# Optimization experiments

Hardware: AMD Instinct MI355X
Metric: run time of the kernel (lower is better)

## Reference

```python
import jax, jax.numpy as jnp
import numpy as np

T, H, E, I, K = 2048, 2048, 8, 2048, 2


def setup_inputs() -> dict:
    key = jax.random.key(0)
    ks = jax.random.split(key, 6)
    s_in = 1.0 / np.sqrt(H)
    s_mid = 1.0 / np.sqrt(I)
    return {
        "hidden_states": jax.random.normal(ks[0], (T, H), jnp.float32),
        "router_logits": jax.random.normal(ks[1], (T, E), jnp.float32),
        "per_expert_scale": jax.random.uniform(ks[2], (E,), jnp.float32, 0.5, 1.5),
        "w_gate": jax.random.normal(ks[3], (E, H, I), jnp.float32) * s_in,
        "w_up": jax.random.normal(ks[4], (E, H, I), jnp.float32) * s_in,
        "w_down": jax.random.normal(ks[5], (E, I, H), jnp.float32) * s_mid,
    }


def _route(router_logits, per_expert_scale):
    # Gemma4 routing: topk over logits, softmax over ALL experts,
    # renormalize over selected experts, fold in per-expert scale.
    _, topk_ids = jax.lax.top_k(router_logits, K)              # [T, K]
    probs = jax.nn.softmax(router_logits, axis=-1)             # [T, E]
    topk_probs = jnp.take_along_axis(probs, topk_ids, axis=-1)  # [T, K]
    renorm = jnp.sum(topk_probs, axis=-1, keepdims=True)
    renorm = jnp.where(renorm > 0.0, renorm, 1.0)
    topk_weights = topk_probs / renorm
    topk_weights = topk_weights * per_expert_scale[topk_ids]
    return topk_weights.astype(jnp.float32), topk_ids.astype(jnp.int32)


def reference(hidden_states, router_logits, per_expert_scale, w_gate, w_up, w_down):
    topk_weights, topk_ids = _route(router_logits, per_expert_scale)
    # dense combine weights [T, E] (zero outside top-k slots)
    combine = jnp.zeros((T, E), jnp.float32)
    combine = combine.at[jnp.arange(T)[:, None], topk_ids].set(topk_weights)
    # gated gelu MLP per expert, dense over experts, weighted combine
    g = jax.nn.gelu(jnp.einsum('th,ehi->tei', hidden_states, w_gate), approximate=True)
    u = jnp.einsum('th,ehi->tei', hidden_states, w_up)
    expert_out = jnp.einsum('tei,eih->teh', g * u, w_down)      # [T, E, H]
    out = jnp.einsum('te,teh->th', combine, expert_out)
    return out
```

## Files before the change

kernel.cpp:

```cpp
#include <hip/hip_runtime.h>
#include <hip/hip_bf16.h>

#define TT 2048
#define HD 2048
#define ID 2048
#define NE 8

typedef __attribute__((ext_vector_type(8))) short short8;
typedef __attribute__((ext_vector_type(4))) float f4;

__device__ __forceinline__ unsigned short b16(float f){
  union { __hip_bfloat16 b; unsigned short u; } x;
  x.b = __float2bfloat16(f);
  return x.u;
}
__device__ __forceinline__ unsigned pk2(float lo, float hi){
  return (unsigned)b16(lo) | ((unsigned)b16(hi) << 16);
}
__device__ __forceinline__ float gelu_t(float x){
  float y = 0.7978845608028654f * (x + 0.044715f * x * x * x);
  float t = 1.0f - 2.0f / (__expf(2.0f * y) + 1.0f);
  return 0.5f * x * (1.0f + t);
}
__device__ __forceinline__ void glds16(const void* g, void* l){
  __builtin_amdgcn_global_load_lds(
      (const __attribute__((address_space(1))) unsigned*)g,
      (__attribute__((address_space(3))) unsigned*)l, 16, 0, 0);
}
__device__ __forceinline__ void softbar(){
  asm volatile("s_waitcnt lgkmcnt(0)" ::: "memory");
  __builtin_amdgcn_s_barrier();
  __builtin_amdgcn_sched_barrier(0);
}
__device__ __forceinline__ int swzB2(int np){ return (((np >> 2) & 7) ^ ((np & 3) << 1)) & 7; }

__global__ void k_cvtx(const float* __restrict__ X, __hip_bfloat16* __restrict__ Xb){
  int i = blockIdx.x * 256 + threadIdx.x;
  const f4* src = (const f4*)X + (size_t)i * 2;
  f4 a = src[0], b = src[1];
  uint4 o = { pk2(a[0],a[1]), pk2(a[2],a[3]), pk2(b[0],b[1]), pk2(b[2],b[3]) };
  ((uint4*)Xb)[i] = o;
}

__global__ void k_route(const float* __restrict__ lg, const float* __restrict__ sc,
                        int* __restrict__ rid, float* __restrict__ rw){
  int t = blockIdx.x * blockDim.x + threadIdx.x;
  if (t >= TT) return;
  float l[NE];
#pragma unroll
  for (int e = 0; e < NE; e++) l[e] = lg[t * NE + e];
  float mx = l[0];
#pragma unroll
  for (int e = 1; e < NE; e++) mx = fmaxf(mx, l[e]);
  float p[NE];
#pragma unroll
  for (int e = 0; e < NE; e++) p[e] = __expf(l[e] - mx);
  int i0 = 0; float b0 = l[0];
#pragma unroll
  for (int e = 1; e < NE; e++) if (l[e] > b0){ b0 = l[e]; i0 = e; }
  int i1 = -1; float b1 = -1e30f;
#pragma unroll
  for (int e = 0; e < NE; e++) if (e != i0 && l[e] > b1){ b1 = l[e]; i1 = e; }
  float p0 = p[i0], p1 = p[i1];
  float rn = p0 + p1; rn = (rn > 0.f) ? rn : 1.f;
  rw[t*2]   = p0 / rn * sc[i0];
  rw[t*2+1] = p1 / rn * sc[i1];
  rid[t*2]  = i0;
  rid[t*2+1]= i1;
}

__global__ void k_lists(const int* __restrict__ rid, const float* __restrict__ rw,
                        int* __restrict__ row_tok, float* __restrict__ row_w,
                        int* __restrict__ off){
  int lane = threadIdx.x;
  int ids[64]; float wv[64];
#pragma unroll
  for (int i = 0; i < 64; i++) ids[i] = rid[i * 64 + lane];
#pragma unroll
  for (int i = 0; i < 64; i++) wv[i] = rw[i * 64 + lane];
  int cnt[NE];
#pragma unroll
  for (int e = 0; e < NE; e++) cnt[e] = 0;
#pragma unroll
  for (int i = 0; i < 64; i++){
#pragma unroll
    for (int e = 0; e < NE; e++)
      cnt[e] += __popcll(__ballot(ids[i] == e));
  }
  int offs[NE + 1]; offs[0] = 0;
#pragma unroll
  for (int e = 0; e < NE; e++) offs[e + 1] = offs[e] + cnt[e];
  if (lane == 0){
#pragma unroll
    for (int e = 0; e <= NE; e++) off[e] = offs[e];
  }
  int run[NE];
#pragma unroll
  for (int e = 0; e < NE; e++) run[e] = offs[e];
  unsigned long long ltm = (1ULL << lane) - 1ULL;
#pragma unroll
  for (int i = 0; i < 64; i++){
    int id = ids[i];
    int tok = (i * 64 + lane) >> 1;
#pragma unroll
    for (int e = 0; e < NE; e++){
      unsigned long long m = __ballot(id == e);
      if (id == e){
        int pos = run[e] + __popcll(m & ltm);
        row_tok[pos] = tok;
        row_w[pos]   = wv[i];
      }
      run[e] += __popcll(m);
    }
  }
}


__global__ __launch_bounds__(256, 3)
void k_gu_f(const __hip_bfloat16* __restrict__ Xb, const float* __restrict__ Wg,
            const float* __restrict__ Wu, const int* __restrict__ row_tok,
            const float* __restrict__ row_w, const int* __restrict__ off,
            __hip_bfloat16* __restrict__ hbuf){
  __shared__ __align__(16) char sA[2][16384];
  __shared__ __align__(16) char sB[16384];
  __shared__ int s_tok[128];
  __shared__ float s_w[128];

  const int bid = blockIdx.x;
  const int e  = bid & 7;
  const int t  = bid >> 3;
  const int mt = t % 5;
  const int nt = t / 5;
  const int o0 = off[e], cnt = off[e + 1] - o0;
  if (mt * 128 >= cnt) return;
  const int p0 = o0 + mt * 128;
  const int cntL = min(128, cnt - mt * 128);
  const int tid = threadIdx.x;
  const int wid = tid >> 6, lane = tid & 63;

  if (tid < 128){
    int p = min(p0 + tid, TT*2 - 1);
    s_tok[tid] = row_tok[p];
    s_w[tid]   = row_w[p];
  }
  __syncthreads();

  const int sw = (((lane & 7) ^ (lane >> 3)) & 7) << 4;
  const char* asrc[4];
#pragma unroll
  for (int i = 0; i < 4; i++){
    int r = (wid * 4 + i) * 8 + (lane >> 3);
    asrc[i] = (const char*)Xb + (size_t)s_tok[r] * 4096 + sw;
  }
  const int m2 = tid >> 7, tt = tid & 127;
  const int n0 = (tt & 15) * 4;
  const int s0 = tt >> 4;
  const float* wsrc = (m2 ? Wu : Wg) + (size_t)e * HD * ID
                    + (size_t)(s0 * 8) * ID + (size_t)nt * 64 + n0;
  int bw[4];
#pragma unroll
  for (int j = 0; j < 4; j++){
    int n  = n0 + j;
    int np = (n >> 5) * 64 + (n & 31) + m2 * 32;
    bw[j] = np * 128 + (((s0 ^ swzB2(np)) & 7) << 4);
  }
  const int wm = wid >> 1, wn = wid & 1;
  const int kg = lane >> 4, ln = lane & 15;
  int aoff[4], boff[4];
#pragma unroll
  for (int f = 0; f < 4; f++){
    int m = wm * 64 + f * 16 + ln;
    aoff[f] = m * 128 + (((kg ^ (m & 7)) & 7) << 4);
    int n = wn * 64 + f * 16 + ln;
    boff[f] = n * 128 + (((kg ^ swzB2(n)) & 7) << 4);
  }

  f4 acc[4][4];
#pragma unroll
  for (int a = 0; a < 4; a++)
#pragma unroll
    for (int b = 0; b < 4; b++) acc[a][b] = f4{0,0,0,0};

#pragma unroll
  for (int i = 0; i < 4; i++) glds16(asrc[i], &sA[0][0] + (wid * 4 + i) * 1024);
  f4 rk[8];
#pragma unroll
  for (int i = 0; i < 8; i++) rk[i] = *(const f4*)(wsrc + (size_t)i * ID);

  for (int kt = 0; kt < 32; ++kt){
    softbar();
#pragma unroll
    for (int j = 0; j < 4; j++){
      *(uint4*)(sB + bw[j]) = uint4{ pk2(rk[0][j], rk[1][j]), pk2(rk[2][j], rk[3][j]),
                                     pk2(rk[4][j], rk[5][j]), pk2(rk[6][j], rk[7][j]) };
    }
    __builtin_amdgcn_sched_barrier(0);
    if (kt + 1 < 32){
      const int _o = (kt + 1) * 128;
      char* dst = &sA[(kt + 1) & 1][0] + (wid * 4) * 1024;
#pragma unroll
      for (int i = 0; i < 4; i++) glds16(asrc[i] + _o, dst + i * 1024);
    }
    __builtin_amdgcn_sched_barrier(0);
    if (kt + 1 < 32){
      const float* p = wsrc + (size_t)(kt + 1) * 64 * ID;
#pragma unroll
      for (int i = 0; i < 8; i++) rk[i] = *(const f4*)(p + (size_t)i * ID);
    }
    __builtin_amdgcn_sched_barrier(0);
    asm volatile("s_waitcnt lgkmcnt(0)" ::: "memory");
    __builtin_amdgcn_s_barrier();
    __builtin_amdgcn_sched_barrier(0);
    const char* A = &sA[kt & 1][0];
#pragma unroll
    for (int ks = 0; ks < 2; ks++){
      const int kx = ks * 64;
      short8 af[4], bf[4];
#pragma unroll
      for (int f = 0; f < 4; f++) af[f] = *(const short8*)(A + (aoff[f] ^ kx));
#pragma unroll
      for (int f = 0; f < 4; f++) bf[f] = *(const short8*)(sB + (boff[f] ^ kx));
#pragma unroll
      for (int fn = 0; fn < 4; fn++)
#pragma unroll
        for (int fm = 0; fm < 4; fm++)
          acc[fm][fn] = __builtin_amdgcn_mfma_f32_16x16x32_bf16(af[fm], bf[fn], acc[fm][fn], 0, 0, 0);
    }
  }
#pragma unroll
  for (int fm = 0; fm < 4; fm++){
#pragma unroll
    for (int r = 0; r < 4; r++){
      int row = wm * 64 + fm * 16 + (lane >> 4) * 4 + r;
      if (row < cntL){
        float w = s_w[row];
        size_t base = (size_t)(p0 + row) * ID + (size_t)nt * 64 + wn * 32 + ln;
#pragma unroll
        for (int fn = 0; fn < 2; fn++){
          float g = acc[fm][fn][r];
          float u = acc[fm][fn + 2][r];
          hbuf[base + fn * 16] = __float2bfloat16(w * gelu_t(g) * u);
        }
      }
    }
  }
}

__global__ __launch_bounds__(256, 3)
void k_dn_f(const __hip_bfloat16* __restrict__ hbuf, const float* __restrict__ Wd,
            const int* __restrict__ row_tok, const int* __restrict__ off,
            float* __restrict__ out){
  __shared__ __align__(16) char sA[2][16384];
  __shared__ __align__(16) char sB[16384];
  __shared__ int s_tok[128];

  const int bid = blockIdx.x;
  const int e  = bid & 7;
  const int t  = bid >> 3;
  const int mt = t % 5;
  const int nt = t / 5;
  const int o0 = off[e], cnt = off[e + 1] - o0;
  if (mt * 128 >= cnt) return;
  const int p0 = o0 + mt * 128;
  const int cntL = min(128, cnt - mt * 128);
  const int tid = threadIdx.x;
  const int wid = tid >> 6, lane = tid & 63;

  if (tid < 128){
    int p = min(p0 + tid, TT*2 - 1);
    s_tok[tid] = row_tok[p];
  }
  __syncthreads();

  const int sw = (((lane & 7) ^ (lane >> 3)) & 7) << 4;
  const char* asrc[4];
#pragma unroll
  for (int i = 0; i < 4; i++){
    int r = (wid * 4 + i) * 8 + (lane >> 3);
    int p = min(p0 + r, TT*2 - 1);
    asrc[i] = (const char*)hbuf + (size_t)p * 4096 + sw;
  }
  const int n0 = (tid & 31) * 4;
  const int s0 = tid >> 5;
  const float* wsrc = Wd + (size_t)e * ID * HD + (size_t)(s0 * 8) * HD + (size_t)nt * 128 + n0;
  int bw[4];
#pragma unroll
  for (int j = 0; j < 4; j++){
    int np = n0 + j;
    bw[j] = np * 128 + (((s0 ^ swzB2(np)) & 7) << 4);
  }
  const int wm = wid >> 1, wn = wid & 1;
  const int kg = lane >> 4, ln = lane & 15;
  int aoff[4], boff[4];
#pragma unroll
  for (int f = 0; f < 4; f++){
    int m = wm * 64 + f * 16 + ln;
    aoff[f] = m * 128 + (((kg ^ (m & 7)) & 7) << 4);
    int n = wn * 64 + f * 16 + ln;
    boff[f] = n * 128 + (((kg ^ swzB2(n)) & 7) << 4);
  }

  f4 acc[4][4];
#pragma unroll
  for (int a = 0; a < 4; a++)
#pragma unroll
    for (int b = 0; b < 4; b++) acc[a][b] = f4{0,0,0,0};

#pragma unroll
  for (int i = 0; i < 4; i++) glds16(asrc[i], &sA[0][0] + (wid * 4 + i) * 1024);
  f4 rk[8];
#pragma unroll
  for (int i = 0; i < 8; i++) rk[i] = *(const f4*)(wsrc + (size_t)i * HD);

  for (int kt = 0; kt < 32; ++kt){
    softbar();
#pragma unroll
    for (int j = 0; j < 4; j++){
      *(uint4*)(sB + bw[j]) = uint4{ pk2(rk[0][j], rk[1][j]), pk2(rk[2][j], rk[3][j]),
                                     pk2(rk[4][j], rk[5][j]), pk2(rk[6][j], rk[7][j]) };
    }
    __builtin_amdgcn_sched_barrier(0);
    if (kt + 1 < 32){
      const int _o = (kt + 1) * 128;
      char* dst = &sA[(kt + 1) & 1][0] + (wid * 4) * 1024;
#pragma unroll
      for (int i = 0; i < 4; i++) glds16(asrc[i] + _o, dst + i * 1024);
    }
    __builtin_amdgcn_sched_barrier(0);
    if (kt + 1 < 32){
      const float* p = wsrc + (size_t)(kt + 1) * 64 * HD;
#pragma unroll
      for (int i = 0; i < 8; i++) rk[i] = *(const f4*)(p + (size_t)i * HD);
    }
    __builtin_amdgcn_sched_barrier(0);
    asm volatile("s_waitcnt lgkmcnt(0)" ::: "memory");
    __builtin_amdgcn_s_barrier();
    __builtin_amdgcn_sched_barrier(0);
    const char* A = &sA[kt & 1][0];
#pragma unroll
    for (int ks = 0; ks < 2; ks++){
      const int kx = ks * 64;
      short8 af[4], bf[4];
#pragma unroll
      for (int f = 0; f < 4; f++) af[f] = *(const short8*)(A + (aoff[f] ^ kx));
#pragma unroll
      for (int f = 0; f < 4; f++) bf[f] = *(const short8*)(sB + (boff[f] ^ kx));
#pragma unroll
      for (int fn = 0; fn < 4; fn++)
#pragma unroll
        for (int fm = 0; fm < 4; fm++)
          acc[fm][fn] = __builtin_amdgcn_mfma_f32_16x16x32_bf16(af[fm], bf[fn], acc[fm][fn], 0, 0, 0);
    }
  }
#pragma unroll
  for (int fm = 0; fm < 4; fm++){
#pragma unroll
    for (int r = 0; r < 4; r++){
      int row = wm * 64 + fm * 16 + (lane >> 4) * 4 + r;
      if (row < cntL){
        int tok = s_tok[row];
        float* ob = out + (size_t)tok * HD + (size_t)nt * 128 + wn * 64 + ln;
#pragma unroll
        for (int fn = 0; fn < 4; fn++)
          atomicAdd(ob + fn * 16, acc[fm][fn][r]);
      }
    }
  }
}

extern "C" void kernel_launch(void* const* d_in, const int* in_sizes, int n_in,
                              void* d_out, int out_size, void* d_ws, size_t ws_size,
                              hipStream_t stream){
  (void)in_sizes; (void)n_in; (void)out_size; (void)ws_size;
  const float* X  = (const float*)d_in[0];
  const float* RL = (const float*)d_in[1];
  const float* SC = (const float*)d_in[2];
  const float* Wg = (const float*)d_in[3];
  const float* Wu = (const float*)d_in[4];
  const float* Wd = (const float*)d_in[5];
  float* out = (float*)d_out;

  char* ws = (char*)d_ws;
  int*   rid     = (int*)(ws);
  float* rw      = (float*)(ws + 16384);
  int*   row_tok = (int*)(ws + 32768);
  float* row_w   = (float*)(ws + 49152);
  int*   off     = (int*)(ws + 65536);
  __hip_bfloat16* hbuf = (__hip_bfloat16*)(ws + 66560);
  __hip_bfloat16* Xb   = (__hip_bfloat16*)(ws + 66560 + 16777216ull);

  hipMemsetAsync(d_out, 0, (size_t)TT * HD * sizeof(float), stream);
  k_cvtx <<<2048, 256, 0, stream>>>(X, Xb);
  k_route<<<TT / 256, 256, 0, stream>>>(RL, SC, rid, rw);
  k_lists<<<1, 64, 0, stream>>>(rid, rw, row_tok, row_w, off);
  k_gu_f<<<1280, 256, 0, stream>>>(Xb, Wg, Wu, row_tok, row_w, off, hbuf);
  k_dn_f<<< 640, 256, 0, stream>>>(hbuf, Wd, row_tok, off, out);
}
```

Before: 302.1 us.

## Make expert GEMM kernels persistent with an atomic tile work queue

Both expert GEMM kernels become persistent. A fixed grid of 768 blocks pulls tile indices from a global atomic counter, which k_lists resets each call, instead of launching one block per potential tile and early-exiting empty ones. This is meant to cut the cost of launching and retiring blocks for empty tiles, and to balance uneven per-expert token counts across CUs. In exchange it adds an atomic and a barrier per tile. The shared s_tile slot can be overwritten by thread 0 before slower waves have read it on the empty-tile path, which risks waves disagreeing on the tile or mismatched barriers.

```diff
diff --git a/kernel.cpp b/kernel.cpp
--- a/kernel.cpp
+++ b/kernel.cpp
@@ -71,8 +71,9 @@
 
 __global__ void k_lists(const int* __restrict__ rid, const float* __restrict__ rw,
                         int* __restrict__ row_tok, float* __restrict__ row_w,
-                        int* __restrict__ off){
+                        int* __restrict__ off, int* __restrict__ qcnt){
   int lane = threadIdx.x;
+  if (lane < 2) qcnt[lane] = 0;
   int ids[64]; float wv[64];
 #pragma unroll
   for (int i = 0; i < 64; i++) ids[i] = rid[i * 64 + lane];
@@ -120,43 +121,20 @@
 void k_gu_f(const __hip_bfloat16* __restrict__ Xb, const float* __restrict__ Wg,
             const float* __restrict__ Wu, const int* __restrict__ row_tok,
             const float* __restrict__ row_w, const int* __restrict__ off,
-            __hip_bfloat16* __restrict__ hbuf){
+            int* __restrict__ qcnt, __hip_bfloat16* __restrict__ hbuf){
   __shared__ __align__(16) char sA[2][16384];
   __shared__ __align__(16) char sB[16384];
   __shared__ int s_tok[128];
   __shared__ float s_w[128];
-
-  const int bid = blockIdx.x;
-  const int e  = bid & 7;
-  const int t  = bid >> 3;
-  const int mt = t % 5;
-  const int nt = t / 5;
-  const int o0 = off[e], cnt = off[e + 1] - o0;
-  if (mt * 128 >= cnt) return;
-  const int p0 = o0 + mt * 128;
-  const int cntL = min(128, cnt - mt * 128);
+  __shared__ int s_tile;
+
   const int tid = threadIdx.x;
   const int wid = tid >> 6, lane = tid & 63;
 
-  if (tid < 128){
-    int p = min(p0 + tid, TT*2 - 1);
-    s_tok[tid] = row_tok[p];
-    s_w[tid]   = row_w[p];
-  }
-  __syncthreads();
-
   const int sw = (((lane & 7) ^ (lane >> 3)) & 7) << 4;
-  const char* asrc[4];
-#pragma unroll
-  for (int i = 0; i < 4; i++){
-    int r = (wid * 4 + i) * 8 + (lane >> 3);
-    asrc[i] = (const char*)Xb + (size_t)s_tok[r] * 4096 + sw;
-  }
   const int m2 = tid >> 7, tt = tid & 127;
   const int n0 = (tt & 15) * 4;
   const int s0 = tt >> 4;
-  const float* wsrc = (m2 ? Wu : Wg) + (size_t)e * HD * ID
-                    + (size_t)(s0 * 8) * ID + (size_t)nt * 64 + n0;
   int bw[4];
 #pragma unroll
   for (int j = 0; j < 4; j++){
@@ -175,71 +153,102 @@
     boff[f] = n * 128 + (((kg ^ swzB2(n)) & 7) << 4);
   }
 
-  f4 acc[4][4];
-#pragma unroll
-  for (int a = 0; a < 4; a++)
-#pragma unroll
-    for (int b = 0; b < 4; b++) acc[a][b] = f4{0,0,0,0};
-
-#pragma unroll
-  for (int i = 0; i < 4; i++) glds16(asrc[i], &sA[0][0] + (wid * 4 + i) * 1024);
-  f4 rk[8];
-#pragma unroll
-  for (int i = 0; i < 8; i++) rk[i] = *(const f4*)(wsrc + (size_t)i * ID);
-
-  for (int kt = 0; kt < 32; ++kt){
-    softbar();
-#pragma unroll
-    for (int j = 0; j < 4; j++){
-      *(uint4*)(sB + bw[j]) = uint4{ pk2(rk[0][j], rk[1][j]), pk2(rk[2][j], rk[3][j]),
-                                     pk2(rk[4][j], rk[5][j]), pk2(rk[6][j], rk[7][j]) };
-    }
-    __builtin_amdgcn_sched_barrier(0);
-    if (kt + 1 < 32){
-      const int _o = (kt + 1) * 128;
-      char* dst = &sA[(kt + 1) & 1][0] + (wid * 4) * 1024;
-#pragma unroll
-      for (int i = 0; i < 4; i++) glds16(asrc[i] + _o, dst + i * 1024);
-    }
-    __builtin_amdgcn_sched_barrier(0);
-    if (kt + 1 < 32){
-      const float* p = wsrc + (size_t)(kt + 1) * 64 * ID;
-#pragma unroll
-      for (int i = 0; i < 8; i++) rk[i] = *(const f4*)(p + (size_t)i * ID);
-    }
-    __builtin_amdgcn_sched_barrier(0);
-    asm volatile("s_waitcnt lgkmcnt(0)" ::: "memory");
-    __builtin_amdgcn_s_barrier();
-    __builtin_amdgcn_sched_barrier(0);
-    const char* A = &sA[kt & 1][0];
-#pragma unroll
-    for (int ks = 0; ks < 2; ks++){
-      const int kx = ks * 64;
-      short8 af[4], bf[4];
-#pragma unroll
-      for (int f = 0; f < 4; f++) af[f] = *(const short8*)(A + (aoff[f] ^ kx));
-#pragma unroll
-      for (int f = 0; f < 4; f++) bf[f] = *(const short8*)(sB + (boff[f] ^ kx));
-#pragma unroll
-      for (int fn = 0; fn < 4; fn++)
-#pragma unroll
-        for (int fm = 0; fm < 4; fm++)
-          acc[fm][fn] = __builtin_amdgcn_mfma_f32_16x16x32_bf16(af[fm], bf[fn], acc[fm][fn], 0, 0, 0);
-    }
-  }
-#pragma unroll
-  for (int fm = 0; fm < 4; fm++){
-#pragma unroll
-    for (int r = 0; r < 4; r++){
-      int row = wm * 64 + fm * 16 + (lane >> 4) * 4 + r;
-      if (row < cntL){
-        float w = s_w[row];
-        size_t base = (size_t)(p0 + row) * ID + (size_t)nt * 64 + wn * 32 + ln;
-#pragma unroll
-        for (int fn = 0; fn < 2; fn++){
-          float g = acc[fm][fn][r];
-          float u = acc[fm][fn + 2][r];
-          hbuf[base + fn * 16] = __float2bfloat16(w * gelu_t(g) * u);
+  for (;;){
+    if (tid == 0) s_tile = atomicAdd(qcnt, 1);
+    __syncthreads();
+    const int tile = s_tile;
+    if (tile >= 1280) break;
+    const int e  = tile & 7;
+    const int t  = tile >> 3;
+    const int mt = t % 5;
+    const int nt = t / 5;
+    const int o0 = off[e], cnt = off[e + 1] - o0;
+    if (mt * 128 >= cnt) continue;
+    const int p0 = o0 + mt * 128;
+    const int cntL = min(128, cnt - mt * 128);
+
+    if (tid < 128){
+      int p = min(p0 + tid, TT*2 - 1);
+      s_tok[tid] = row_tok[p];
+      s_w[tid]   = row_w[p];
+    }
+    __syncthreads();
+
+    const char* asrc[4];
+#pragma unroll
+    for (int i = 0; i < 4; i++){
+      int r = (wid * 4 + i) * 8 + (lane >> 3);
+      asrc[i] = (const char*)Xb + (size_t)s_tok[r] * 4096 + sw;
+    }
+    const float* wsrc = (m2 ? Wu : Wg) + (size_t)e * HD * ID
+                      + (size_t)(s0 * 8) * ID + (size_t)nt * 64 + n0;
+
+    f4 acc[4][4];
+#pragma unroll
+    for (int a = 0; a < 4; a++)
+#pragma unroll
+      for (int b = 0; b < 4; b++) acc[a][b] = f4{0,0,0,0};
+
+#pragma unroll
+    for (int i = 0; i < 4; i++) glds16(asrc[i], &sA[0][0] + (wid * 4 + i) * 1024);
+    f4 rk[8];
+#pragma unroll
+    for (int i = 0; i < 8; i++) rk[i] = *(const f4*)(wsrc + (size_t)i * ID);
+
+    for (int kt = 0; kt < 32; ++kt){
+      softbar();
+#pragma unroll
+      for (int j = 0; j < 4; j++){
+        *(uint4*)(sB + bw[j]) = uint4{ pk2(rk[0][j], rk[1][j]), pk2(rk[2][j], rk[3][j]),
+                                       pk2(rk[4][j], rk[5][j]), pk2(rk[6][j], rk[7][j]) };
+      }
+      __builtin_amdgcn_sched_barrier(0);
+      if (kt + 1 < 32){
+        const int _o = (kt + 1) * 128;
+        char* dst = &sA[(kt + 1) & 1][0] + (wid * 4) * 1024;
+#pragma unroll
+        for (int i = 0; i < 4; i++) glds16(asrc[i] + _o, dst + i * 1024);
+      }
+      __builtin_amdgcn_sched_barrier(0);
+      if (kt + 1 < 32){
+        const float* p = wsrc + (size_t)(kt + 1) * 64 * ID;
+#pragma unroll
+        for (int i = 0; i < 8; i++) rk[i] = *(const f4*)(p + (size_t)i * ID);
+      }
+      __builtin_amdgcn_sched_barrier(0);
+      asm volatile("s_waitcnt lgkmcnt(0)" ::: "memory");
+      __builtin_amdgcn_s_barrier();
+      __builtin_amdgcn_sched_barrier(0);
+      const char* A = &sA[kt & 1][0];
+#pragma unroll
+      for (int ks = 0; ks < 2; ks++){
+        const int kx = ks * 64;
+        short8 af[4], bf[4];
+#pragma unroll
+        for (int f = 0; f < 4; f++) af[f] = *(const short8*)(A + (aoff[f] ^ kx));
+#pragma unroll
+        for (int f = 0; f < 4; f++) bf[f] = *(const short8*)(sB + (boff[f] ^ kx));
+#pragma unroll
+        for (int fn = 0; fn < 4; fn++)
+#pragma unroll
+          for (int fm = 0; fm < 4; fm++)
+            acc[fm][fn] = __builtin_amdgcn_mfma_f32_16x16x32_bf16(af[fm], bf[fn], acc[fm][fn], 0, 0, 0);
+      }
+    }
+#pragma unroll
+    for (int fm = 0; fm < 4; fm++){
+#pragma unroll
+      for (int r = 0; r < 4; r++){
+        int row = wm * 64 + fm * 16 + (lane >> 4) * 4 + r;
+        if (row < cntL){
+          float w = s_w[row];
+          size_t base = (size_t)(p0 + row) * ID + (size_t)nt * 64 + wn * 32 + ln;
+#pragma unroll
+          for (int fn = 0; fn < 2; fn++){
+            float g = acc[fm][fn][r];
+            float u = acc[fm][fn + 2][r];
+            hbuf[base + fn * 16] = __float2bfloat16(w * gelu_t(g) * u);
+          }
         }
       }
     }
@@ -249,40 +258,18 @@
 __global__ __launch_bounds__(256, 3)
 void k_dn_f(const __hip_bfloat16* __restrict__ hbuf, const float* __restrict__ Wd,
             const int* __restrict__ row_tok, const int* __restrict__ off,
-            float* __restrict__ out){
+            int* __restrict__ qcnt, float* __restrict__ out){
   __shared__ __align__(16) char sA[2][16384];
   __shared__ __align__(16) char sB[16384];
   __shared__ int s_tok[128];
-
-  const int bid = blockIdx.x;
-  const int e  = bid & 7;
-  const int t  = bid >> 3;
-  const int mt = t % 5;
-  const int nt = t / 5;
-  const int o0 = off[e], cnt = off[e + 1] - o0;
-  if (mt * 128 >= cnt) return;
-  const int p0 = o0 + mt * 128;
-  const int cntL = min(128, cnt - mt * 128);
+  __shared__ int s_tile;
+
   const int tid = threadIdx.x;
   const int wid = tid >> 6, lane = tid & 63;
 
-  if (tid < 128){
-    int p = min(p0 + tid, TT*2 - 1);
-    s_tok[tid] = row_tok[p];
-  }
-  __syncthreads();
-
   const int sw = (((lane & 7) ^ (lane >> 3)) & 7) << 4;
-  const char* asrc[4];
-#pragma unroll
-  for (int i = 0; i < 4; i++){
-    int r = (wid * 4 + i) * 8 + (lane >> 3);
-    int p = min(p0 + r, TT*2 - 1);
-    asrc[i] = (const char*)hbuf + (size_t)p * 4096 + sw;
-  }
   const int n0 = (tid & 31) * 4;
   const int s0 = tid >> 5;
-  const float* wsrc = Wd + (size_t)e * ID * HD + (size_t)(s0 * 8) * HD + (size_t)nt * 128 + n0;
   int bw[4];
 #pragma unroll
   for (int j = 0; j < 4; j++){
@@ -300,69 +287,99 @@
     boff[f] = n * 128 + (((kg ^ swzB2(n)) & 7) << 4);
   }
 
-  f4 acc[4][4];
-#pragma unroll
-  for (int a = 0; a < 4; a++)
-#pragma unroll
-    for (int b = 0; b < 4; b++) acc[a][b] = f4{0,0,0,0};
-
-#pragma unroll
-  for (int i = 0; i < 4; i++) glds16(asrc[i], &sA[0][0] + (wid * 4 + i) * 1024);
-  f4 rk[8];
-#pragma unroll
-  for (int i = 0; i < 8; i++) rk[i] = *(const f4*)(wsrc + (size_t)i * HD);
-
-  for (int kt = 0; kt < 32; ++kt){
-    softbar();
-#pragma unroll
-    for (int j = 0; j < 4; j++){
-      *(uint4*)(sB + bw[j]) = uint4{ pk2(rk[0][j], rk[1][j]), pk2(rk[2][j], rk[3][j]),
-                                     pk2(rk[4][j], rk[5][j]), pk2(rk[6][j], rk[7][j]) };
-    }
-    __builtin_amdgcn_sched_barrier(0);
-    if (kt + 1 < 32){
-      const int _o = (kt + 1) * 128;
-      char* dst = &sA[(kt + 1) & 1][0] + (wid * 4) * 1024;
-#pragma unroll
-      for (int i = 0; i < 4; i++) glds16(asrc[i] + _o, dst + i * 1024);
-    }
-    __builtin_amdgcn_sched_barrier(0);
-    if (kt + 1 < 32){
-      const float* p = wsrc + (size_t)(kt + 1) * 64 * HD;
-#pragma unroll
-      for (int i = 0; i < 8; i++) rk[i] = *(const f4*)(p + (size_t)i * HD);
-    }
-    __builtin_amdgcn_sched_barrier(0);
-    asm volatile("s_waitcnt lgkmcnt(0)" ::: "memory");
-    __builtin_amdgcn_s_barrier();
-    __builtin_amdgcn_sched_barrier(0);
-    const char* A = &sA[kt & 1][0];
-#pragma unroll
-    for (int ks = 0; ks < 2; ks++){
-      const int kx = ks * 64;
-      short8 af[4], bf[4];
-#pragma unroll
-      for (int f = 0; f < 4; f++) af[f] = *(const short8*)(A + (aoff[f] ^ kx));
-#pragma unroll
-      for (int f = 0; f < 4; f++) bf[f] = *(const short8*)(sB + (boff[f] ^ kx));
-#pragma unroll
-      for (int fn = 0; fn < 4; fn++)
-#pragma unroll
-        for (int fm = 0; fm < 4; fm++)
-          acc[fm][fn] = __builtin_amdgcn_mfma_f32_16x16x32_bf16(af[fm], bf[fn], acc[fm][fn], 0, 0, 0);
-    }
-  }
-#pragma unroll
-  for (int fm = 0; fm < 4; fm++){
-#pragma unroll
-    for (int r = 0; r < 4; r++){
-      int row = wm * 64 + fm * 16 + (lane >> 4) * 4 + r;
-      if (row < cntL){
-        int tok = s_tok[row];
-        float* ob = out + (size_t)tok * HD + (size_t)nt * 128 + wn * 64 + ln;
+  for (;;){
+    if (tid == 0) s_tile = atomicAdd(qcnt + 1, 1);
+    __syncthreads();
+    const int tile = s_tile;
+    if (tile >= 640) break;
+    const int e  = tile & 7;
+    const int t  = tile >> 3;
+    const int mt = t % 5;
+    const int nt = t / 5;
+    const int o0 = off[e], cnt = off[e + 1] - o0;
+    if (mt * 128 >= cnt) continue;
+    const int p0 = o0 + mt * 128;
+    const int cntL = min(128, cnt - mt * 128);
+
+    if (tid < 128){
+      int p = min(p0 + tid, TT*2 - 1);
+      s_tok[tid] = row_tok[p];
+    }
+    __syncthreads();
+
+    const char* asrc[4];
+#pragma unroll
+    for (int i = 0; i < 4; i++){
+      int r = (wid * 4 + i) * 8 + (lane >> 3);
+      int p = min(p0 + r, TT*2 - 1);
+      asrc[i] = (const char*)hbuf + (size_t)p * 4096 + sw;
+    }
+    const float* wsrc = Wd + (size_t)e * ID * HD + (size_t)(s0 * 8) * HD + (size_t)nt * 128 + n0;
+
+    f4 acc[4][4];
+#pragma unroll
+    for (int a = 0; a < 4; a++)
+#pragma unroll
+      for (int b = 0; b < 4; b++) acc[a][b] = f4{0,0,0,0};
+
+#pragma unroll
+    for (int i = 0; i < 4; i++) glds16(asrc[i], &sA[0][0] + (wid * 4 + i) * 1024);
+    f4 rk[8];
+#pragma unroll
+    for (int i = 0; i < 8; i++) rk[i] = *(const f4*)(wsrc + (size_t)i * HD);
+
+    for (int kt = 0; kt < 32; ++kt){
+      softbar();
+#pragma unroll
+      for (int j = 0; j < 4; j++){
+        *(uint4*)(sB + bw[j]) = uint4{ pk2(rk[0][j], rk[1][j]), pk2(rk[2][j], rk[3][j]),
+                                       pk2(rk[4][j], rk[5][j]), pk2(rk[6][j], rk[7][j]) };
+      }
+      __builtin_amdgcn_sched_barrier(0);
+      if (kt + 1 < 32){
+        const int _o = (kt + 1) * 128;
+        char* dst = &sA[(kt + 1) & 1][0] + (wid * 4) * 1024;
+#pragma unroll
+        for (int i = 0; i < 4; i++) glds16(asrc[i] + _o, dst + i * 1024);
+      }
+      __builtin_amdgcn_sched_barrier(0);
+      if (kt + 1 < 32){
+        const float* p = wsrc + (size_t)(kt + 1) * 64 * HD;
+#pragma unroll
+        for (int i = 0; i < 8; i++) rk[i] = *(const f4*)(p + (size_t)i * HD);
+      }
+      __builtin_amdgcn_sched_barrier(0);
+      asm volatile("s_waitcnt lgkmcnt(0)" ::: "memory");
+      __builtin_amdgcn_s_barrier();
+      __builtin_amdgcn_sched_barrier(0);
+      const char* A = &sA[kt & 1][0];
+#pragma unroll
+      for (int ks = 0; ks < 2; ks++){
+        const int kx = ks * 64;
+        short8 af[4], bf[4];
+#pragma unroll
+        for (int f = 0; f < 4; f++) af[f] = *(const short8*)(A + (aoff[f] ^ kx));
+#pragma unroll
+        for (int f = 0; f < 4; f++) bf[f] = *(const short8*)(sB + (boff[f] ^ kx));
 #pragma unroll
         for (int fn = 0; fn < 4; fn++)
-          atomicAdd(ob + fn * 16, acc[fm][fn][r]);
+#pragma unroll
+          for (int fm = 0; fm < 4; fm++)
+            acc[fm][fn] = __builtin_amdgcn_mfma_f32_16x16x32_bf16(af[fm], bf[fn], acc[fm][fn], 0, 0, 0);
+      }
+    }
+#pragma unroll
+    for (int fm = 0; fm < 4; fm++){
+#pragma unroll
+      for (int r = 0; r < 4; r++){
+        int row = wm * 64 + fm * 16 + (lane >> 4) * 4 + r;
+        if (row < cntL){
+          int tok = s_tok[row];
+          float* ob = out + (size_t)tok * HD + (size_t)nt * 128 + wn * 64 + ln;
+#pragma unroll
+          for (int fn = 0; fn < 4; fn++)
+            atomicAdd(ob + fn * 16, acc[fm][fn][r]);
+        }
       }
     }
   }
@@ -386,13 +403,14 @@
   int*   row_tok = (int*)(ws + 32768);
   float* row_w   = (float*)(ws + 49152);
   int*   off     = (int*)(ws + 65536);
+  int*   qcnt    = (int*)(ws + 66048);
   __hip_bfloat16* hbuf = (__hip_bfloat16*)(ws + 66560);
   __hip_bfloat16* Xb   = (__hip_bfloat16*)(ws + 66560 + 16777216ull);
 
   hipMemsetAsync(d_out, 0, (size_t)TT * HD * sizeof(float), stream);
   k_cvtx <<<2048, 256, 0, stream>>>(X, Xb);
   k_route<<<TT / 256, 256, 0, stream>>>(RL, SC, rid, rw);
-  k_lists<<<1, 64, 0, stream>>>(rid, rw, row_tok, row_w, off);
-  k_gu_f<<<1280, 256, 0, stream>>>(Xb, Wg, Wu, row_tok, row_w, off, hbuf);
-  k_dn_f<<< 640, 256, 0, stream>>>(hbuf, Wd, row_tok, off, out);
-}
+  k_lists<<<1, 64, 0, stream>>>(rid, rw, row_tok, row_w, off, qcnt);
+  k_gu_f<<<768, 256, 0, stream>>>(Xb, Wg, Wu, row_tok, row_w, off, qcnt, hbuf);
+  k_dn_f<<<768, 256, 0, stream>>>(hbuf, Wd, row_tok, off, qcnt, out);
+}
```

Result: slower. 396.9 us (+31.4%).

## Double the M tile to 256 rows and single-buffer the activation tile

Applied to the files above, without the earlier changes.

Both expert GEMM kernels now cover 256 routed rows per block instead of 128, with 8x4 MFMA fragments per wave. Each expert needs 3 M tiles instead of 5, so the fp32 expert weights are read and converted to bf16 fewer times. The double-buffered A tile becomes one 32 KB buffer, loaded at the start of each k-step and waited on with a partial vmcnt that leaves the weight prefetch in flight. The costs are higher register pressure (launch bounds drop from 3 to 2 blocks per SM), less overlap of A loads with compute, and rows lost if any expert receives more than 768 assignments.

```diff
diff --git a/kernel.cpp b/kernel.cpp
--- a/kernel.cpp
+++ b/kernel.cpp
@@ -116,29 +116,29 @@
 }
 
 
-__global__ __launch_bounds__(256, 3)
+__global__ __launch_bounds__(256, 2)
 void k_gu_f(const __hip_bfloat16* __restrict__ Xb, const float* __restrict__ Wg,
             const float* __restrict__ Wu, const int* __restrict__ row_tok,
             const float* __restrict__ row_w, const int* __restrict__ off,
             __hip_bfloat16* __restrict__ hbuf){
-  __shared__ __align__(16) char sA[2][16384];
+  __shared__ __align__(16) char sA[32768];
   __shared__ __align__(16) char sB[16384];
-  __shared__ int s_tok[128];
-  __shared__ float s_w[128];
+  __shared__ int s_tok[256];
+  __shared__ float s_w[256];
 
   const int bid = blockIdx.x;
   const int e  = bid & 7;
   const int t  = bid >> 3;
-  const int mt = t % 5;
-  const int nt = t / 5;
+  const int mt = t % 3;
+  const int nt = t / 3;
   const int o0 = off[e], cnt = off[e + 1] - o0;
-  if (mt * 128 >= cnt) return;
-  const int p0 = o0 + mt * 128;
-  const int cntL = min(128, cnt - mt * 128);
+  if (mt * 256 >= cnt) return;
+  const int p0 = o0 + mt * 256;
+  const int cntL = min(256, cnt - mt * 256);
   const int tid = threadIdx.x;
   const int wid = tid >> 6, lane = tid & 63;
 
-  if (tid < 128){
+  {
     int p = min(p0 + tid, TT*2 - 1);
     s_tok[tid] = row_tok[p];
     s_w[tid]   = row_w[p];
@@ -146,10 +146,10 @@
   __syncthreads();
 
   const int sw = (((lane & 7) ^ (lane >> 3)) & 7) << 4;
-  const char* asrc[4];
-#pragma unroll
-  for (int i = 0; i < 4; i++){
-    int r = (wid * 4 + i) * 8 + (lane >> 3);
+  const char* asrc[8];
+#pragma unroll
+  for (int i = 0; i < 8; i++){
+    int r = (wid * 8 + i) * 8 + (lane >> 3);
     asrc[i] = (const char*)Xb + (size_t)s_tok[r] * 4096 + sw;
   }
   const int m2 = tid >> 7, tt = tid & 127;
@@ -166,29 +166,36 @@
   }
   const int wm = wid >> 1, wn = wid & 1;
   const int kg = lane >> 4, ln = lane & 15;
-  int aoff[4], boff[4];
+  int aoff[8], boff[4];
+#pragma unroll
+  for (int f = 0; f < 8; f++){
+    int m = wm * 128 + f * 16 + ln;
+    aoff[f] = m * 128 + (((kg ^ (m & 7)) & 7) << 4);
+  }
 #pragma unroll
   for (int f = 0; f < 4; f++){
-    int m = wm * 64 + f * 16 + ln;
-    aoff[f] = m * 128 + (((kg ^ (m & 7)) & 7) << 4);
     int n = wn * 64 + f * 16 + ln;
     boff[f] = n * 128 + (((kg ^ swzB2(n)) & 7) << 4);
   }
 
-  f4 acc[4][4];
-#pragma unroll
-  for (int a = 0; a < 4; a++)
+  f4 acc[8][4];
+#pragma unroll
+  for (int a = 0; a < 8; a++)
 #pragma unroll
     for (int b = 0; b < 4; b++) acc[a][b] = f4{0,0,0,0};
 
-#pragma unroll
-  for (int i = 0; i < 4; i++) glds16(asrc[i], &sA[0][0] + (wid * 4 + i) * 1024);
   f4 rk[8];
 #pragma unroll
   for (int i = 0; i < 8; i++) rk[i] = *(const f4*)(wsrc + (size_t)i * ID);
+  __builtin_amdgcn_sched_barrier(0);
 
   for (int kt = 0; kt < 32; ++kt){
     softbar();
+    { const int _o = kt * 128;
+#pragma unroll
+      for (int i = 0; i < 8; i++) glds16(asrc[i] + _o, sA + (wid * 8 + i) * 1024);
+    }
+    __builtin_amdgcn_sched_barrier(0);
 #pragma unroll
     for (int j = 0; j < 4; j++){
       *(uint4*)(sB + bw[j]) = uint4{ pk2(rk[0][j], rk[1][j]), pk2(rk[2][j], rk[3][j]),
@@ -196,42 +203,38 @@
     }
     __builtin_amdgcn_sched_barrier(0);
     if (kt + 1 < 32){
-      const int _o = (kt + 1) * 128;
-      char* dst = &sA[(kt + 1) & 1][0] + (wid * 4) * 1024;
-#pragma unroll
-      for (int i = 0; i < 4; i++) glds16(asrc[i] + _o, dst + i * 1024);
+      const float* p = wsrc + (size_t)(kt + 1) * 64 * ID;
+#pragma unroll
+      for (int i = 0; i < 8; i++) rk[i] = *(const f4*)(p + (size_t)i * ID);
     }
     __builtin_amdgcn_sched_barrier(0);
     if (kt + 1 < 32){
-      const float* p = wsrc + (size_t)(kt + 1) * 64 * ID;
-#pragma unroll
-      for (int i = 0; i < 8; i++) rk[i] = *(const f4*)(p + (size_t)i * ID);
-    }
-    __builtin_amdgcn_sched_barrier(0);
-    asm volatile("s_waitcnt lgkmcnt(0)" ::: "memory");
+      asm volatile("s_waitcnt vmcnt(8) lgkmcnt(0)" ::: "memory");
+    } else {
+      asm volatile("s_waitcnt vmcnt(0) lgkmcnt(0)" ::: "memory");
+    }
     __builtin_amdgcn_s_barrier();
     __builtin_amdgcn_sched_barrier(0);
-    const char* A = &sA[kt & 1][0];
 #pragma unroll
     for (int ks = 0; ks < 2; ks++){
       const int kx = ks * 64;
-      short8 af[4], bf[4];
-#pragma unroll
-      for (int f = 0; f < 4; f++) af[f] = *(const short8*)(A + (aoff[f] ^ kx));
+      short8 bf[4];
 #pragma unroll
       for (int f = 0; f < 4; f++) bf[f] = *(const short8*)(sB + (boff[f] ^ kx));
 #pragma unroll
-      for (int fn = 0; fn < 4; fn++)
-#pragma unroll
-        for (int fm = 0; fm < 4; fm++)
-          acc[fm][fn] = __builtin_amdgcn_mfma_f32_16x16x32_bf16(af[fm], bf[fn], acc[fm][fn], 0, 0, 0);
-    }
-  }
-#pragma unroll
-  for (int fm = 0; fm < 4; fm++){
+      for (int fm = 0; fm < 8; fm++){
+        short8 af = *(const short8*)(sA + (aoff[fm] ^ kx));
+#pragma unroll
+        for (int fn = 0; fn < 4; fn++)
+          acc[fm][fn] = __builtin_amdgcn_mfma_f32_16x16x32_bf16(af, bf[fn], acc[fm][fn], 0, 0, 0);
+      }
+    }
+  }
+#pragma unroll
+  for (int fm = 0; fm < 8; fm++){
 #pragma unroll
     for (int r = 0; r < 4; r++){
-      int row = wm * 64 + fm * 16 + (lane >> 4) * 4 + r;
+      int row = wm * 128 + fm * 16 + (lane >> 4) * 4 + r;
       if (row < cntL){
         float w = s_w[row];
         size_t base = (size_t)(p0 + row) * ID + (size_t)nt * 64 + wn * 32 + ln;
@@ -246,39 +249,38 @@
   }
 }
 
-__global__ __launch_bounds__(256, 3)
+__global__ __launch_bounds__(256, 2)
 void k_dn_f(const __hip_bfloat16* __restrict__ hbuf, const float* __restrict__ Wd,
             const int* __restrict__ row_tok, const int* __restrict__ off,
             float* __restrict__ out){
-  __shared__ __align__(16) char sA[2][16384];
+  __shared__ __align__(16) char sA[32768];
   __shared__ __align__(16) char sB[16384];
-  __shared__ int s_tok[128];
+  __shared__ int s_tok[256];
 
   const int bid = blockIdx.x;
   const int e  = bid & 7;
   const int t  = bid >> 3;
-  const int mt = t % 5;
-  const int nt = t / 5;
+  const int mt = t % 3;
+  const int nt = t / 3;
   const int o0 = off[e], cnt = off[e + 1] - o0;
-  if (mt * 128 >= cnt) return;
-  const int p0 = o0 + mt * 128;
-  const int cntL = min(128, cnt - mt * 128);
+  if (mt * 256 >= cnt) return;
+  const int p0 = o0 + mt * 256;
+  const int cntL = min(256, cnt - mt * 256);
   const int tid = threadIdx.x;
   const int wid = tid >> 6, lane = tid & 63;
 
-  if (tid < 128){
+  {
     int p = min(p0 + tid, TT*2 - 1);
     s_tok[tid] = row_tok[p];
   }
   __syncthreads();
 
   const int sw = (((lane & 7) ^ (lane >> 3)) & 7) << 4;
-  const char* asrc[4];
-#pragma unroll
-  for (int i = 0; i < 4; i++){
-    int r = (wid * 4 + i) * 8 + (lane >> 3);
-    int p = min(p0 + r, TT*2 - 1);
-    asrc[i] = (const char*)hbuf + (size_t)p * 4096 + sw;
+  const char* asrc[8];
+#pragma unroll
+  for (int i = 0; i < 8; i++){
+    int r = (wid * 8 + i) * 8 + (lane >> 3);
+    asrc[i] = (const char*)hbuf + (size_t)s_tok[r] * 0 + (size_t)min(p0 + r, TT*2 - 1) * 4096 + sw;
   }
   const int n0 = (tid & 31) * 4;
   const int s0 = tid >> 5;
@@ -291,29 +293,36 @@
   }
   const int wm = wid >> 1, wn = wid & 1;
   const int kg = lane >> 4, ln = lane & 15;
-  int aoff[4], boff[4];
+  int aoff[8], boff[4];
+#pragma unroll
+  for (int f = 0; f < 8; f++){
+    int m = wm * 128 + f * 16 + ln;
+    aoff[f] = m * 128 + (((kg ^ (m & 7)) & 7) << 4);
+  }
 #pragma unroll
   for (int f = 0; f < 4; f++){
-    int m = wm * 64 + f * 16 + ln;
-    aoff[f] = m * 128 + (((kg ^ (m & 7)) & 7) << 4);
     int n = wn * 64 + f * 16 + ln;
     boff[f] = n * 128 + (((kg ^ swzB2(n)) & 7) << 4);
   }
 
-  f4 acc[4][4];
-#pragma unroll
-  for (int a = 0; a < 4; a++)
+  f4 acc[8][4];
+#pragma unroll
+  for (int a = 0; a < 8; a++)
 #pragma unroll
     for (int b = 0; b < 4; b++) acc[a][b] = f4{0,0,0,0};
 
-#pragma unroll
-  for (int i = 0; i < 4; i++) glds16(asrc[i], &sA[0][0] + (wid * 4 + i) * 1024);
   f4 rk[8];
 #pragma unroll
   for (int i = 0; i < 8; i++) rk[i] = *(const f4*)(wsrc + (size_t)i * HD);
+  __builtin_amdgcn_sched_barrier(0);
 
   for (int kt = 0; kt < 32; ++kt){
     softbar();
+    { const int _o = kt * 128;
+#pragma unroll
+      for (int i = 0; i < 8; i++) glds16(asrc[i] + _o, sA + (wid * 8 + i) * 1024);
+    }
+    __builtin_amdgcn_sched_barrier(0);
 #pragma unroll
     for (int j = 0; j < 4; j++){
       *(uint4*)(sB + bw[j]) = uint4{ pk2(rk[0][j], rk[1][j]), pk2(rk[2][j], rk[3][j]),
@@ -321,42 +330,38 @@
     }
     __builtin_amdgcn_sched_barrier(0);
     if (kt + 1 < 32){
-      const int _o = (kt + 1) * 128;
-      char* dst = &sA[(kt + 1) & 1][0] + (wid * 4) * 1024;
-#pragma unroll
-      for (int i = 0; i < 4; i++) glds16(asrc[i] + _o, dst + i * 1024);
+      const float* p = wsrc + (size_t)(kt + 1) * 64 * HD;
+#pragma unroll
+      for (int i = 0; i < 8; i++) rk[i] = *(const f4*)(p + (size_t)i * HD);
     }
     __builtin_amdgcn_sched_barrier(0);
     if (kt + 1 < 32){
-      const float* p = wsrc + (size_t)(kt + 1) * 64 * HD;
-#pragma unroll
-      for (int i = 0; i < 8; i++) rk[i] = *(const f4*)(p + (size_t)i * HD);
-    }
-    __builtin_amdgcn_sched_barrier(0);
-    asm volatile("s_waitcnt lgkmcnt(0)" ::: "memory");
+      asm volatile("s_waitcnt vmcnt(8) lgkmcnt(0)" ::: "memory");
+    } else {
+      asm volatile("s_waitcnt vmcnt(0) lgkmcnt(0)" ::: "memory");
+    }
     __builtin_amdgcn_s_barrier();
     __builtin_amdgcn_sched_barrier(0);
-    const char* A = &sA[kt & 1][0];
 #pragma unroll
     for (int ks = 0; ks < 2; ks++){
       const int kx = ks * 64;
-      short8 af[4], bf[4];
-#pragma unroll
-      for (int f = 0; f < 4; f++) af[f] = *(const short8*)(A + (aoff[f] ^ kx));
+      short8 bf[4];
 #pragma unroll
       for (int f = 0; f < 4; f++) bf[f] = *(const short8*)(sB + (boff[f] ^ kx));
 #pragma unroll
-      for (int fn = 0; fn < 4; fn++)
-#pragma unroll
-        for (int fm = 0; fm < 4; fm++)
-          acc[fm][fn] = __builtin_amdgcn_mfma_f32_16x16x32_bf16(af[fm], bf[fn], acc[fm][fn], 0, 0, 0);
-    }
-  }
-#pragma unroll
-  for (int fm = 0; fm < 4; fm++){
+      for (int fm = 0; fm < 8; fm++){
+        short8 af = *(const short8*)(sA + (aoff[fm] ^ kx));
+#pragma unroll
+        for (int fn = 0; fn < 4; fn++)
+          acc[fm][fn] = __builtin_amdgcn_mfma_f32_16x16x32_bf16(af, bf[fn], acc[fm][fn], 0, 0, 0);
+      }
+    }
+  }
+#pragma unroll
+  for (int fm = 0; fm < 8; fm++){
 #pragma unroll
     for (int r = 0; r < 4; r++){
-      int row = wm * 64 + fm * 16 + (lane >> 4) * 4 + r;
+      int row = wm * 128 + fm * 16 + (lane >> 4) * 4 + r;
       if (row < cntL){
         int tok = s_tok[row];
         float* ob = out + (size_t)tok * HD + (size_t)nt * 128 + wn * 64 + ln;
@@ -393,6 +398,6 @@
   k_cvtx <<<2048, 256, 0, stream>>>(X, Xb);
   k_route<<<TT / 256, 256, 0, stream>>>(RL, SC, rid, rw);
   k_lists<<<1, 64, 0, stream>>>(rid, rw, row_tok, row_w, off);
-  k_gu_f<<<1280, 256, 0, stream>>>(Xb, Wg, Wu, row_tok, row_w, off, hbuf);
-  k_dn_f<<< 640, 256, 0, stream>>>(hbuf, Wd, row_tok, off, out);
-}
+  k_gu_f<<<768, 256, 0, stream>>>(Xb, Wg, Wu, row_tok, row_w, off, hbuf);
+  k_dn_f<<<384, 256, 0, stream>>>(hbuf, Wd, row_tok, off, out);
+}
```

New measurement: 324.9 us. +7.6%, slower.
